# Optimization experiments

Hardware: AMD Instinct MI355X
Metric: run time of the kernel (lower is better)

## Reference

```python
import jax, jax.numpy as jnp
import numpy as np

FX = FY = 100.0
UX = UY = 48.0
Z_RANGE = 1.0  # __init__ hardcodes self.z_range = 1 regardless of the arg


def setup_inputs() -> dict:
    key = jax.random.key(0)
    k1, k2, k3, k4, k5 = jax.random.split(key, 5)
    B = 4
    voxels = jax.random.normal(k1, (B, 32, 64, 64, 64), jnp.float32)
    # proper per-batch rotations embedded in 4x4 homogeneous matrices
    m = np.asarray(jax.random.normal(k2, (B, 3, 3)), dtype=np.float64)
    q, _ = np.linalg.qr(m)
    q = q * np.sign(np.linalg.det(q))[:, None, None]
    rot = np.tile(np.eye(4, dtype=np.float32), (B, 1, 1))
    rot[:, :3, :3] = q.astype(np.float32)
    rot = jnp.asarray(rot)
    # translation: small xy offset, z ~ 1 so the sampled slab lands in view
    tran = jnp.concatenate([0.1 * jax.random.normal(k3, (B, 2)),
                            jnp.ones((B, 1))], axis=-1).astype(jnp.float32)
    s = jax.random.uniform(k4, (B, 3), jnp.float32, 0.8, 1.2)
    det = 2.0 * jax.random.normal(k5, (B, 2), jnp.float32)
    return {"voxels": voxels, "rot": rot, "tran": tran, "s": s, "det": det,
            "xy_sample": 96, "z_sample": 48}


def camera2world(rot, tran, s):
    B = rot.shape[0]
    rotT = jnp.swapaxes(rot[:, :3, :3], 1, 2)                      # R^T  [B,3,3]
    t_inv = -jnp.einsum('bij,bj->bi', rotT, tran)                  # -R^T t [B,3]
    top = jnp.concatenate([rotT, t_inv[..., None]], axis=-1)       # [B,3,4]
    bottom = jnp.broadcast_to(jnp.array([0., 0., 0., 1.], rot.dtype), (B, 1, 4))
    rt_inv = jnp.concatenate([top, bottom], axis=1)                # [B,4,4]
    diag = jnp.concatenate([1.0 / s, jnp.ones((B, 1), s.dtype)], axis=-1)
    scale_inv = jax.vmap(jnp.diag)(diag)                           # [B,4,4]
    return jnp.matmul(scale_inv, rt_inv)


def ray2grid(tran, det, xy_sample, z_sample):
    # torch.linspace(0, width, width): endpoints 0..width with `width` points
    x_t = jnp.linspace(0.0, xy_sample, xy_sample, dtype=jnp.float32)
    y_t = jnp.linspace(0.0, xy_sample, xy_sample, dtype=jnp.float32)
    z_t = jnp.linspace(-Z_RANGE / 2, Z_RANGE / 2, z_sample, dtype=jnp.float32)
    zz, yy, xx = jnp.meshgrid(z_t, y_t, x_t, indexing='ij')        # [Z,H,W]
    tz = tran[:, 2][:, None, None, None]
    dx = det[:, 0][:, None, None, None]
    dy = det[:, 1][:, None, None, None]
    Zt = zz[None] + tz                                             # [B,Z,H,W]
    Xt = (xx[None] - UX + dx) * Zt / FX
    Yt = (yy[None] - UY + dy) * Zt / FY
    ones = jnp.ones_like(Xt)
    return jnp.stack([Xt, Yt, Zt, ones], axis=-1)                  # [B,Z,H,W,4]


def grid_sample_3d(vox, grid):
    # vox [B,C,D,H,W], grid [B,Do,Ho,Wo,3] in (x,y,z) normalized coords,
    # trilinear, zeros padding, align_corners=True
    B, C, D, H, W = vox.shape
    voxc = jnp.moveaxis(vox, 1, -1)                                # [B,D,H,W,C]
    ix = (grid[..., 0] + 1.0) * 0.5 * (W - 1)
    iy = (grid[..., 1] + 1.0) * 0.5 * (H - 1)
    iz = (grid[..., 2] + 1.0) * 0.5 * (D - 1)
    ix0, iy0, iz0 = jnp.floor(ix), jnp.floor(iy), jnp.floor(iz)
    fx, fy, fz = ix - ix0, iy - iy0, iz - iz0
    bidx = jnp.arange(B)[:, None, None, None]
    out = jnp.zeros(grid.shape[:-1] + (C,), vox.dtype)
    for dz in (0, 1):
        wz = fz if dz else 1.0 - fz
        zi = iz0 + dz
        for dy in (0, 1):
            wy = fy if dy else 1.0 - fy
            yi = iy0 + dy
            for dx in (0, 1):
                wx = fx if dx else 1.0 - fx
                xi = ix0 + dx
                valid = ((xi >= 0) & (xi <= W - 1) & (yi >= 0) & (yi <= H - 1)
                         & (zi >= 0) & (zi <= D - 1))
                xc = jnp.clip(xi, 0, W - 1).astype(jnp.int32)
                yc = jnp.clip(yi, 0, H - 1).astype(jnp.int32)
                zc = jnp.clip(zi, 0, D - 1).astype(jnp.int32)
                w = (wz * wy * wx) * valid.astype(vox.dtype)
                out = out + w[..., None] * voxc[bidx, zc, yc, xc]
    return jnp.moveaxis(out, -1, 1)                                # [B,C,Do,Ho,Wo]


def reference(voxels, rot, tran, s, det, xy_sample, z_sample):
    wTc = camera2world(rot, tran, s)                               # [B,4,4]
    cGrid = ray2grid(tran, det, xy_sample, z_sample)               # [B,Z,H,W,4]
    wGrid = jnp.einsum('bzhwk,bjk->bzhwj', cGrid, wTc)             # cGrid @ wTc^T
    wGrid = 2.0 * wGrid[..., 0:3] / wGrid[..., 3:4]
    return grid_sample_3d(voxels, wGrid)
```

## Files before the change

kernel.cpp:

```cpp
#include <hip/hip_runtime.h>
#include <hip/hip_fp16.h>


static constexpr int Bn = 4, Cn = 32, DV = 64, HV = 64, WV = 64;
static constexpr int ZS = 48, XY = 96;
static constexpr int SP = ZS * XY * XY;
static constexpr long long VOXCH = (long long)DV * HV * WV;
static constexpr size_t WS_NEED = (size_t)Bn * VOXCH * Cn * sizeof(__half);

static __device__ __forceinline__ unsigned pk2h(float a, float b) {
    __half2 h2;
    h2.x = __float2half(a);
    h2.y = __float2half(b);
    return *reinterpret_cast<unsigned*>(&h2);
}

__global__ __launch_bounds__(256) void transpose_cl(
    const float* __restrict__ vox, __half* __restrict__ voxt)
{
    __shared__ float tile[32][65];
    const int nt = (int)(VOXCH / 64);
    const int blk = blockIdx.x;
    const int b  = blk / nt;
    const int v0 = (blk - b * nt) * 64;
    const int t  = threadIdx.x;
    {
        const int c = t >> 3;
        const int i = (t & 7) * 8;
        const float* src = vox + ((size_t)(b * Cn + c)) * VOXCH + v0 + i;
        const float4 a0 = *(const float4*)src;
        const float4 a1 = *(const float4*)(src + 4);
        tile[c][i + 0] = a0.x; tile[c][i + 1] = a0.y;
        tile[c][i + 2] = a0.z; tile[c][i + 3] = a0.w;
        tile[c][i + 4] = a1.x; tile[c][i + 5] = a1.y;
        tile[c][i + 6] = a1.z; tile[c][i + 7] = a1.w;
    }
    __syncthreads();
    {
        const int v  = t >> 2;
        const int c8 = (t & 3) * 8;
        const unsigned p0 = pk2h(tile[c8 + 0][v], tile[c8 + 1][v]);
        const unsigned p1 = pk2h(tile[c8 + 2][v], tile[c8 + 3][v]);
        const unsigned p2 = pk2h(tile[c8 + 4][v], tile[c8 + 5][v]);
        const unsigned p3 = pk2h(tile[c8 + 6][v], tile[c8 + 7][v]);
        __half* dst = voxt + ((size_t)b * VOXCH + v0 + v) * Cn + c8;
        *(uint4*)dst = make_uint4(p0, p1, p2, p3);
    }
}

static constexpr int NBLK2 = Bn * ZS * XY;
static constexpr int CH2   = NBLK2 / 8;

__global__ __launch_bounds__(192) void sample_cl(
    const __half* __restrict__ voxt,
    const float* __restrict__ rot,
    const float* __restrict__ tran,
    const float* __restrict__ sc,
    const float* __restrict__ det,
    float* __restrict__ out)
{
    __shared__ __align__(16) int   soff[96][8];
    __shared__ __align__(16) float swt[96][8];
    __shared__ float tr[3][32][34];

    const int logical = (blockIdx.x % 8) * CH2 + blockIdx.x / 8;
    const int b   = logical / (ZS * XY);
    const int rem = logical - b * (ZS * XY);
    const int z   = rem / XY;
    const int h   = rem - z * XY;

    const int t = threadIdx.x;

    if (t < XY) {
        const float* R  = rot  + b * 16;
        const float* T  = tran + b * 3;
        const float* S  = sc   + b * 3;
        const float* DT = det  + b * 2;
        const float t0 = T[0], t1 = T[1], t2 = T[2];

        float M[3][4];
#pragma unroll
        for (int i2 = 0; i2 < 3; ++i2) {
            const float inv = 1.0f / S[i2];
            const float m0 = R[0 * 4 + i2], m1 = R[1 * 4 + i2], m2 = R[2 * 4 + i2];
            M[i2][0] = inv * m0;
            M[i2][1] = inv * m1;
            M[i2][2] = inv * m2;
            M[i2][3] = -inv * (m0 * t0 + m1 * t1 + m2 * t2);
        }

        const float STEP = 96.0f / 95.0f;
        const float Zt = -0.5f + z * (1.0f / 47.0f) + t2;
        const float Xt = (t * STEP - 48.0f + DT[0]) * Zt * 0.01f;
        const float Yt = (h * STEP - 48.0f + DT[1]) * Zt * 0.01f;

        const float gx = 2.0f * (M[0][0] * Xt + M[0][1] * Yt + M[0][2] * Zt + M[0][3]);
        const float gy = 2.0f * (M[1][0] * Xt + M[1][1] * Yt + M[1][2] * Zt + M[1][3]);
        const float gz = 2.0f * (M[2][0] * Xt + M[2][1] * Yt + M[2][2] * Zt + M[2][3]);

        const float ix = (gx + 1.0f) * 31.5f;
        const float iy = (gy + 1.0f) * 31.5f;
        const float iz = (gz + 1.0f) * 31.5f;

        const float fxf = floorf(ix), fyf = floorf(iy), fzf = floorf(iz);
        const float fx = ix - fxf, fy = iy - fyf, fz = iz - fzf;
        const int x0 = (int)fxf, y0 = (int)fyf, z0 = (int)fzf;

        const float ax0 = (1.0f - fx) * ((x0 >= 0     && x0 < WV)     ? 1.0f : 0.0f);
        const float ax1 = fx          * ((x0 + 1 >= 0 && x0 + 1 < WV) ? 1.0f : 0.0f);
        const float ay0 = (1.0f - fy) * ((y0 >= 0     && y0 < HV)     ? 1.0f : 0.0f);
        const float ay1 = fy          * ((y0 + 1 >= 0 && y0 + 1 < HV) ? 1.0f : 0.0f);
        const float az0 = (1.0f - fz) * ((z0 >= 0     && z0 < DV)     ? 1.0f : 0.0f);
        const float az1 = fz          * ((z0 + 1 >= 0 && z0 + 1 < DV) ? 1.0f : 0.0f);

        const int xc0 = min(max(x0, 0), WV - 1), xc1 = min(max(x0 + 1, 0), WV - 1);
        const int yc0 = min(max(y0, 0), HV - 1), yc1 = min(max(y0 + 1, 0), HV - 1);
        const int zc0 = min(max(z0, 0), DV - 1), zc1 = min(max(z0 + 1, 0), DV - 1);

        const int r00 = (zc0 * HV + yc0) * WV;
        const int r01 = (zc0 * HV + yc1) * WV;
        const int r10 = (zc1 * HV + yc0) * WV;
        const int r11 = (zc1 * HV + yc1) * WV;

        soff[t][0] = (r00 + xc0) << 6;
        soff[t][1] = (r00 + xc1) << 6;
        soff[t][2] = (r01 + xc0) << 6;
        soff[t][3] = (r01 + xc1) << 6;
        soff[t][4] = (r10 + xc0) << 6;
        soff[t][5] = (r10 + xc1) << 6;
        soff[t][6] = (r11 + xc0) << 6;
        soff[t][7] = (r11 + xc1) << 6;

        const float wz0y0 = az0 * ay0, wz0y1 = az0 * ay1;
        const float wz1y0 = az1 * ay0, wz1y1 = az1 * ay1;
        swt[t][0] = wz0y0 * ax0;
        swt[t][1] = wz0y0 * ax1;
        swt[t][2] = wz0y1 * ax0;
        swt[t][3] = wz0y1 * ax1;
        swt[t][4] = wz1y0 * ax0;
        swt[t][5] = wz1y0 * ax1;
        swt[t][6] = wz1y1 * ax0;
        swt[t][7] = wz1y1 * ax1;
    }
    __syncthreads();

    const int wave = t >> 6;
    const int lane = t & 63;
    const int sg   = lane >> 4;
    const int li   = lane & 15;
    const int w0   = wave * 32;
    const int lb   = li * 4;

    const char* vb = (const char*)voxt + (size_t)b * VOXCH * (Cn * 2);

#pragma unroll
    for (int i = 0; i < 8; ++i) {
        const int s  = w0 + 4 * i + sg;
        const int sl = s & 31;
        const int4   o0 = *(const int4*)(&soff[s][0]);
        const int4   o1 = *(const int4*)(&soff[s][4]);
        const float4 wa = *(const float4*)(&swt[s][0]);
        const float4 wb = *(const float4*)(&swt[s][4]);

        const float2 f0 = __half22float2(*(const __half2*)(vb + (o0.x + lb)));
        const float2 f1 = __half22float2(*(const __half2*)(vb + (o0.y + lb)));
        const float2 f2 = __half22float2(*(const __half2*)(vb + (o0.z + lb)));
        const float2 f3 = __half22float2(*(const __half2*)(vb + (o0.w + lb)));
        const float2 f4 = __half22float2(*(const __half2*)(vb + (o1.x + lb)));
        const float2 f5 = __half22float2(*(const __half2*)(vb + (o1.y + lb)));
        const float2 f6 = __half22float2(*(const __half2*)(vb + (o1.z + lb)));
        const float2 f7 = __half22float2(*(const __half2*)(vb + (o1.w + lb)));

        float acc0 = wa.x * f0.x;
        float acc1 = wa.x * f0.y;
        acc0 = fmaf(wa.y, f1.x, acc0); acc1 = fmaf(wa.y, f1.y, acc1);
        acc0 = fmaf(wa.z, f2.x, acc0); acc1 = fmaf(wa.z, f2.y, acc1);
        acc0 = fmaf(wa.w, f3.x, acc0); acc1 = fmaf(wa.w, f3.y, acc1);
        acc0 = fmaf(wb.x, f4.x, acc0); acc1 = fmaf(wb.x, f4.y, acc1);
        acc0 = fmaf(wb.y, f5.x, acc0); acc1 = fmaf(wb.y, f5.y, acc1);
        acc0 = fmaf(wb.z, f6.x, acc0); acc1 = fmaf(wb.z, f6.y, acc1);
        acc0 = fmaf(wb.w, f7.x, acc0); acc1 = fmaf(wb.w, f7.y, acc1);

        *(float2*)(&tr[wave][sl][li * 2]) = make_float2(acc0, acc1);
    }

    __syncthreads();

    const size_t obase = (size_t)b * Cn * SP + (size_t)(z * XY + h) * XY + w0;
    const int p  = lane >> 5;
    const int wl = lane & 31;
#pragma unroll
    for (int c2 = 0; c2 < 16; ++c2) {
        const int cc = 2 * c2 + p;
        __builtin_nontemporal_store(tr[wave][wl][cc],
                                    out + obase + (size_t)cc * SP + wl);
    }
}

static constexpr int TW = 32, TH = 4, TZ = 2;
static constexpr int NBW = XY / TW, NBH = XY / TH, NBZ = ZS / TZ;
static constexpr int BLOCKS_PER_B = NBW * NBH * NBZ;
static constexpr int NBLOCKS = Bn * BLOCKS_PER_B;
static constexpr int CHUNK = NBLOCKS / 8;

__global__ __launch_bounds__(256) void persp3d_fallback(
    const float* __restrict__ vox, const float* __restrict__ rot,
    const float* __restrict__ tran, const float* __restrict__ sc,
    const float* __restrict__ det, float* __restrict__ out)
{
    const int xcd = blockIdx.x % 8;
    const int logical = xcd * CHUNK + blockIdx.x / 8;
    const int b = logical / BLOCKS_PER_B;
    int rem = logical - b * BLOCKS_PER_B;
    const int bz = rem / (NBH * NBW);
    rem -= bz * (NBH * NBW);
    const int bh = rem / NBW;
    const int bw = rem - bh * NBW;
    const int t = threadIdx.x;
    const int w = bw * TW + (t & (TW - 1));
    const int h = bh * TH + ((t >> 5) & (TH - 1));
    const int z = bz * TZ + (t >> 7);
    const int sp = (z * XY + h) * XY + w;

    const float* R = rot + b * 16;
    const float* T = tran + b * 3;
    const float* S = sc + b * 3;
    const float* DT = det + b * 2;
    const float t0 = T[0], t1 = T[1], t2 = T[2];
    float M[3][4];
#pragma unroll
    for (int i = 0; i < 3; ++i) {
        const float inv = 1.0f / S[i];
        const float m0 = R[0 * 4 + i], m1 = R[1 * 4 + i], m2 = R[2 * 4 + i];
        M[i][0] = inv * m0; M[i][1] = inv * m1; M[i][2] = inv * m2;
        M[i][3] = -inv * (m0 * t0 + m1 * t1 + m2 * t2);
    }
    const float STEP = 96.0f / 95.0f;
    const float Zt = -0.5f + z * (1.0f / 47.0f) + t2;
    const float Xt = (w * STEP - 48.0f + DT[0]) * Zt * 0.01f;
    const float Yt = (h * STEP - 48.0f + DT[1]) * Zt * 0.01f;
    const float gx = 2.0f * (M[0][0] * Xt + M[0][1] * Yt + M[0][2] * Zt + M[0][3]);
    const float gy = 2.0f * (M[1][0] * Xt + M[1][1] * Yt + M[1][2] * Zt + M[1][3]);
    const float gz = 2.0f * (M[2][0] * Xt + M[2][1] * Yt + M[2][2] * Zt + M[2][3]);
    const float ix = (gx + 1.0f) * 31.5f, iy = (gy + 1.0f) * 31.5f, iz = (gz + 1.0f) * 31.5f;
    const float fx0 = floorf(ix), fy0 = floorf(iy), fz0 = floorf(iz);
    const float fx = ix - fx0, fy = iy - fy0, fz = iz - fz0;
    const int x0 = (int)fx0, y0 = (int)fy0, z0 = (int)fz0;
    const float ax0 = (1.0f - fx) * ((x0 >= 0 && x0 < WV) ? 1.0f : 0.0f);
    const float ax1 = fx * ((x0 + 1 >= 0 && x0 + 1 < WV) ? 1.0f : 0.0f);
    const float ay0 = (1.0f - fy) * ((y0 >= 0 && y0 < HV) ? 1.0f : 0.0f);
    const float ay1 = fy * ((y0 + 1 >= 0 && y0 + 1 < HV) ? 1.0f : 0.0f);
    const float az0 = (1.0f - fz) * ((z0 >= 0 && z0 < DV) ? 1.0f : 0.0f);
    const float az1 = fz * ((z0 + 1 >= 0 && z0 + 1 < DV) ? 1.0f : 0.0f);
    const int xc0 = min(max(x0, 0), WV - 1), xc1 = min(max(x0 + 1, 0), WV - 1);
    const int yc0 = min(max(y0, 0), HV - 1), yc1 = min(max(y0 + 1, 0), HV - 1);
    const int zc0 = min(max(z0, 0), DV - 1), zc1 = min(max(z0 + 1, 0), DV - 1);
    const int o000 = (zc0 * HV + yc0) * WV + xc0, o001 = (zc0 * HV + yc0) * WV + xc1;
    const int o010 = (zc0 * HV + yc1) * WV + xc0, o011 = (zc0 * HV + yc1) * WV + xc1;
    const int o100 = (zc1 * HV + yc0) * WV + xc0, o101 = (zc1 * HV + yc0) * WV + xc1;
    const int o110 = (zc1 * HV + yc1) * WV + xc0, o111 = (zc1 * HV + yc1) * WV + xc1;
    const float* p = vox + (size_t)b * Cn * VOXCH;
    float* op = out + (size_t)b * Cn * SP + sp;
#pragma unroll 8
    for (int cc = 0; cc < Cn; ++cc) {
        const float v000 = p[o000], v001 = p[o001];
        const float v010 = p[o010], v011 = p[o011];
        const float v100 = p[o100], v101 = p[o101];
        const float v110 = p[o110], v111 = p[o111];
        const float q00 = ax0 * v000 + ax1 * v001;
        const float q01 = ax0 * v010 + ax1 * v011;
        const float q10 = ax0 * v100 + ax1 * v101;
        const float q11 = ax0 * v110 + ax1 * v111;
        const float r0 = ay0 * q00 + ay1 * q01;
        const float r1 = ay0 * q10 + ay1 * q11;
        __builtin_nontemporal_store(az0 * r0 + az1 * r1, op);
        p += VOXCH; op += SP;
    }
}

extern "C" void kernel_launch(void* const* d_in, const int* in_sizes, int n_in,
                              void* d_out, int out_size, void* d_ws, size_t ws_size,
                              hipStream_t stream) {
    const float* vox  = (const float*)d_in[0];
    const float* rot  = (const float*)d_in[1];
    const float* tran = (const float*)d_in[2];
    const float* sc   = (const float*)d_in[3];
    const float* det  = (const float*)d_in[4];
    float* out = (float*)d_out;

    if (ws_size >= WS_NEED) {
        __half* voxt = (__half*)d_ws;
        transpose_cl<<<dim3(Bn * (int)(VOXCH / 64)), dim3(256), 0, stream>>>(vox, voxt);
        sample_cl<<<dim3(NBLK2), dim3(192), 0, stream>>>(voxt, rot, tran, sc, det, out);
    } else {
        persp3d_fallback<<<dim3(NBLOCKS), dim3(256), 0, stream>>>(vox, rot, tran, sc, det, out);
    }
}
```

Measured before the change: 90.30 us.

## Make sampling waves self-contained, drop block barriers, vectorize output stores

Each wave now computes the offsets and weights for its own 32 output columns in per-wave shared memory, which removes both __syncthreads in the sampling kernel. The staging tile is transposed so each lane writes 16-byte nontemporal float4 stores instead of scalar stores. The transpose kernel's input reads become nontemporal loads and the gather loop unroll drops to 4. The cross-lane shared-memory handoff now relies on implicit wavefront lockstep with no explicit barrier, which is a correctness risk if the compiler reorders LDS accesses.

```diff
diff --git a/kernel.cpp b/kernel.cpp
--- a/kernel.cpp
+++ b/kernel.cpp
@@ -1,6 +1,8 @@
 #include <hip/hip_runtime.h>
 #include <hip/hip_fp16.h>
 
+
+typedef float f32x4 __attribute__((ext_vector_type(4)));
 
 static constexpr int Bn = 4, Cn = 32, DV = 64, HV = 64, WV = 64;
 static constexpr int ZS = 48, XY = 96;
@@ -28,8 +30,8 @@
         const int c = t >> 3;
         const int i = (t & 7) * 8;
         const float* src = vox + ((size_t)(b * Cn + c)) * VOXCH + v0 + i;
-        const float4 a0 = *(const float4*)src;
-        const float4 a1 = *(const float4*)(src + 4);
+        const f32x4 a0 = __builtin_nontemporal_load((const f32x4*)src);
+        const f32x4 a1 = __builtin_nontemporal_load((const f32x4*)(src + 4));
         tile[c][i + 0] = a0.x; tile[c][i + 1] = a0.y;
         tile[c][i + 2] = a0.z; tile[c][i + 3] = a0.w;
         tile[c][i + 4] = a1.x; tile[c][i + 5] = a1.y;
@@ -59,9 +61,9 @@
     const float* __restrict__ det,
     float* __restrict__ out)
 {
-    __shared__ __align__(16) int   soff[96][8];
-    __shared__ __align__(16) float swt[96][8];
-    __shared__ float tr[3][32][34];
+    __shared__ __align__(16) int   soff[3][32][8];
+    __shared__ __align__(16) float swt[3][32][8];
+    __shared__ __align__(16) float tr2[3][32][36];
 
     const int logical = (blockIdx.x % 8) * CH2 + blockIdx.x / 8;
     const int b   = logical / (ZS * XY);
@@ -69,9 +71,13 @@
     const int z   = rem / XY;
     const int h   = rem - z * XY;
 
-    const int t = threadIdx.x;
-
-    if (t < XY) {
+    const int t    = threadIdx.x;
+    const int wave = t >> 6;
+    const int lane = t & 63;
+    const int w0   = wave * 32;
+
+    if (lane < 32) {
+        const int w = w0 + lane;
         const float* R  = rot  + b * 16;
         const float* T  = tran + b * 3;
         const float* S  = sc   + b * 3;
@@ -91,7 +97,7 @@
 
         const float STEP = 96.0f / 95.0f;
         const float Zt = -0.5f + z * (1.0f / 47.0f) + t2;
-        const float Xt = (t * STEP - 48.0f + DT[0]) * Zt * 0.01f;
+        const float Xt = (w * STEP - 48.0f + DT[0]) * Zt * 0.01f;
         const float Yt = (h * STEP - 48.0f + DT[1]) * Zt * 0.01f;
 
         const float gx = 2.0f * (M[0][0] * Xt + M[0][1] * Yt + M[0][2] * Zt + M[0][3]);
@@ -122,45 +128,40 @@
         const int r10 = (zc1 * HV + yc0) * WV;
         const int r11 = (zc1 * HV + yc1) * WV;
 
-        soff[t][0] = (r00 + xc0) << 6;
-        soff[t][1] = (r00 + xc1) << 6;
-        soff[t][2] = (r01 + xc0) << 6;
-        soff[t][3] = (r01 + xc1) << 6;
-        soff[t][4] = (r10 + xc0) << 6;
-        soff[t][5] = (r10 + xc1) << 6;
-        soff[t][6] = (r11 + xc0) << 6;
-        soff[t][7] = (r11 + xc1) << 6;
+        soff[wave][lane][0] = (r00 + xc0) << 6;
+        soff[wave][lane][1] = (r00 + xc1) << 6;
+        soff[wave][lane][2] = (r01 + xc0) << 6;
+        soff[wave][lane][3] = (r01 + xc1) << 6;
+        soff[wave][lane][4] = (r10 + xc0) << 6;
+        soff[wave][lane][5] = (r10 + xc1) << 6;
+        soff[wave][lane][6] = (r11 + xc0) << 6;
+        soff[wave][lane][7] = (r11 + xc1) << 6;
 
         const float wz0y0 = az0 * ay0, wz0y1 = az0 * ay1;
         const float wz1y0 = az1 * ay0, wz1y1 = az1 * ay1;
-        swt[t][0] = wz0y0 * ax0;
-        swt[t][1] = wz0y0 * ax1;
-        swt[t][2] = wz0y1 * ax0;
-        swt[t][3] = wz0y1 * ax1;
-        swt[t][4] = wz1y0 * ax0;
-        swt[t][5] = wz1y0 * ax1;
-        swt[t][6] = wz1y1 * ax0;
-        swt[t][7] = wz1y1 * ax1;
-    }
-    __syncthreads();
-
-    const int wave = t >> 6;
-    const int lane = t & 63;
-    const int sg   = lane >> 4;
-    const int li   = lane & 15;
-    const int w0   = wave * 32;
-    const int lb   = li * 4;
+        swt[wave][lane][0] = wz0y0 * ax0;
+        swt[wave][lane][1] = wz0y0 * ax1;
+        swt[wave][lane][2] = wz0y1 * ax0;
+        swt[wave][lane][3] = wz0y1 * ax1;
+        swt[wave][lane][4] = wz1y0 * ax0;
+        swt[wave][lane][5] = wz1y0 * ax1;
+        swt[wave][lane][6] = wz1y1 * ax0;
+        swt[wave][lane][7] = wz1y1 * ax1;
+    }
+
+    const int sg = lane >> 4;
+    const int li = lane & 15;
+    const int lb = li * 4;
 
     const char* vb = (const char*)voxt + (size_t)b * VOXCH * (Cn * 2);
 
-#pragma unroll
+#pragma unroll 4
     for (int i = 0; i < 8; ++i) {
-        const int s  = w0 + 4 * i + sg;
-        const int sl = s & 31;
-        const int4   o0 = *(const int4*)(&soff[s][0]);
-        const int4   o1 = *(const int4*)(&soff[s][4]);
-        const float4 wa = *(const float4*)(&swt[s][0]);
-        const float4 wb = *(const float4*)(&swt[s][4]);
+        const int sl = 4 * i + sg;
+        const int4   o0 = *(const int4*)(&soff[wave][sl][0]);
+        const int4   o1 = *(const int4*)(&soff[wave][sl][4]);
+        const float4 wa = *(const float4*)(&swt[wave][sl][0]);
+        const float4 wb = *(const float4*)(&swt[wave][sl][4]);
 
         const float2 f0 = __half22float2(*(const __half2*)(vb + (o0.x + lb)));
         const float2 f1 = __half22float2(*(const __half2*)(vb + (o0.y + lb)));
@@ -181,19 +182,18 @@
         acc0 = fmaf(wb.z, f6.x, acc0); acc1 = fmaf(wb.z, f6.y, acc1);
         acc0 = fmaf(wb.w, f7.x, acc0); acc1 = fmaf(wb.w, f7.y, acc1);
 
-        *(float2*)(&tr[wave][sl][li * 2]) = make_float2(acc0, acc1);
-    }
-
-    __syncthreads();
-
-    const size_t obase = (size_t)b * Cn * SP + (size_t)(z * XY + h) * XY + w0;
-    const int p  = lane >> 5;
-    const int wl = lane & 31;
+        tr2[wave][2 * li + 0][sl] = acc0;
+        tr2[wave][2 * li + 1][sl] = acc1;
+    }
+
+    const size_t orow = (size_t)b * Cn * SP + (size_t)(z * XY + h) * XY + w0;
+    const int cb = lane >> 3;
+    const int w4 = (lane & 7) * 4;
 #pragma unroll
-    for (int c2 = 0; c2 < 16; ++c2) {
-        const int cc = 2 * c2 + p;
-        __builtin_nontemporal_store(tr[wave][wl][cc],
-                                    out + obase + (size_t)cc * SP + wl);
+    for (int c2 = 0; c2 < 4; ++c2) {
+        const int cc = c2 * 8 + cb;
+        const f32x4 v = *(const f32x4*)(&tr2[wave][cc][w4]);
+        __builtin_nontemporal_store(v, (f32x4*)(out + orow + (size_t)cc * SP + w4));
     }
 }
 
```

New measurement: 102.2 us. +13.2%, slower.
